# Kernel optimization log

Hardware: AMD Instinct MI355X
Metric: run time of the kernel (lower is better)

Reference implementation:

```python
import jax, jax.numpy as jnp
import numpy as np

N_NODES = 100000
N_EDGES = 1600000
D_IN = 128
D_HID = 64
BN_EPS = 1e-5


def setup_inputs() -> dict:
    key = jax.random.key(0)
    ks = jax.random.split(key, 8)
    x = jax.random.normal(ks[0], (N_NODES, D_IN), dtype=jnp.float32)
    edge_index = jax.random.randint(ks[1], (2, N_EDGES), 0, N_NODES, dtype=jnp.int64)
    # GCNConv1 weight/bias (glorot-ish scale)
    W1 = jax.random.normal(ks[2], (D_IN, D_HID), dtype=jnp.float32) / np.sqrt(D_IN)
    b1 = jnp.zeros((D_HID,), dtype=jnp.float32)
    # BatchNorm1d (eval mode: running stats)
    gamma = jax.random.normal(ks[3], (D_HID,), dtype=jnp.float32) * 0.1 + 1.0
    beta = jax.random.normal(ks[4], (D_HID,), dtype=jnp.float32) * 0.1
    run_mean = jnp.zeros((D_HID,), dtype=jnp.float32)
    run_var = jnp.ones((D_HID,), dtype=jnp.float32)
    # fc1: Linear(2*hidden, 2)
    Wfc = jax.random.normal(ks[5], (2 * D_HID, 2), dtype=jnp.float32) / np.sqrt(2 * D_HID)
    bfc = jnp.zeros((2,), dtype=jnp.float32)
    return {"x": x, "edge_index": edge_index, "W1": W1, "b1": b1,
            "gamma": gamma, "beta": beta, "run_mean": run_mean, "run_var": run_var,
            "Wfc": Wfc, "bfc": bfc}


def gcn_conv(x, edge_index, W, b):
    # PyG GCNConv: add self-loops, symmetric normalization, scatter-add aggregation
    n = x.shape[0]
    loops = jnp.arange(n, dtype=edge_index.dtype)
    row = jnp.concatenate([edge_index[0], loops])  # source nodes
    col = jnp.concatenate([edge_index[1], loops])  # target nodes
    deg = jax.ops.segment_sum(jnp.ones_like(col, dtype=x.dtype), col, num_segments=n)
    dinv = jax.lax.rsqrt(jnp.maximum(deg, 1.0))  # deg >= 1 due to self-loops
    norm = dinv[row] * dinv[col]                 # [E+N]
    h = x @ W                                    # [N, hid]
    msgs = h[row] * norm[:, None]                # gather + scale  [E+N, hid]
    out = jax.ops.segment_sum(msgs, col, num_segments=n)  # scatter-add
    return out + b


def reference(x, edge_index, W1, b1, gamma, beta, run_mean, run_var, Wfc, bfc):
    h = gcn_conv(x, edge_index, W1, b1)
    h = jax.nn.relu(h)
    # dropout(p=0.9) is identity in eval mode
    # BatchNorm1d eval: normalize with running stats
    h = (h - run_mean) * jax.lax.rsqrt(run_var + BN_EPS) * gamma + beta
    h = jax.nn.relu(h)
    # edge gather-concat-linear
    er = jnp.concatenate([h[edge_index[0]], h[edge_index[1]]], axis=1)  # [E, 2*hid]
    return er @ Wfc + bfc  # [E, 2]
```

## Files before the change

### kernel.cpp

```cpp
#include <hip/hip_runtime.h>

#define N_NODES 100000
#define N_EDGES 1600000
#define D_IN 128
#define D_HID 64
#define BN_EPS 1e-5f

#define BUCKET_SHIFT 7
#define BUCKET_W 128
#define N_BUCKETS ((N_NODES + BUCKET_W - 1) / BUCKET_W)
#define N_BIN_BLOCKS 256
#define EDGES_PER_BLOCK (N_EDGES / N_BIN_BLOCKS)
#define GT 2

typedef __attribute__((ext_vector_type(8))) short bf16x8;
typedef __attribute__((ext_vector_type(4))) float f32x4;
typedef __attribute__((ext_vector_type(2))) _Float16 f16x2;
typedef __attribute__((ext_vector_type(4))) _Float16 f16x4;

__device__ __forceinline__ ushort f2bf(float f) {
    unsigned u = __float_as_uint(f);
    u += 0x7FFF + ((u >> 16) & 1);
    return (ushort)(u >> 16);
}

__global__ __launch_bounds__(256) void bin_count_kernel(const int* __restrict__ col,
                                                        int* __restrict__ bcount,
                                                        int* __restrict__ bhist) {
    __shared__ int hist[N_BUCKETS];
    const int t = threadIdx.x;
    for (int i = t; i < N_BUCKETS; i += 256) hist[i] = 0;
    __syncthreads();
    const int e0 = blockIdx.x * EDGES_PER_BLOCK;
    for (int j = t; j < EDGES_PER_BLOCK; j += 256)
        atomicAdd(&hist[col[e0 + j] >> BUCKET_SHIFT], 1);
    __syncthreads();
    for (int i = t; i < N_BUCKETS; i += 256) {
        int h = hist[i];
        bhist[blockIdx.x * N_BUCKETS + i] = h;
        if (h) atomicAdd(&bcount[i], h);
    }
}

__global__ __launch_bounds__(1024) void scan_buckets_kernel(const int* __restrict__ bcount,
                                                            int* __restrict__ bstart,
                                                            int* __restrict__ bcursor,
                                                            int* __restrict__ row_start) {
    __shared__ int tmp[1024];
    int t = threadIdx.x;
    int val = (t < N_BUCKETS) ? bcount[t] : 0;
    tmp[t] = val;
    for (int off = 1; off < 1024; off <<= 1) {
        __syncthreads();
        int add = (t >= off) ? tmp[t - off] : 0;
        __syncthreads();
        tmp[t] += add;
    }
    __syncthreads();
    if (t < N_BUCKETS) {
        int s = tmp[t] - val;
        bstart[t] = s;
        bcursor[t] = s;
    }
    if (t == N_BUCKETS - 1) {
        bstart[N_BUCKETS] = tmp[t];
        row_start[N_NODES] = tmp[t];
    }
}

__global__ __launch_bounds__(256) void bin_scatter_kernel(const int* __restrict__ row,
                                                          const int* __restrict__ col,
                                                          const int* __restrict__ bhist,
                                                          int* __restrict__ bcursor,
                                                          int* __restrict__ binned) {
    __shared__ int hist[N_BUCKETS];
    __shared__ int lbase[N_BUCKETS];
    const int t = threadIdx.x;
    for (int i = t; i < N_BUCKETS; i += 256) {
        int h = bhist[blockIdx.x * N_BUCKETS + i];
        lbase[i] = h ? atomicAdd(&bcursor[i], h) : 0;
        hist[i] = 0;
    }
    __syncthreads();
    const int e0 = blockIdx.x * EDGES_PER_BLOCK;
    for (int j = t; j < EDGES_PER_BLOCK; j += 256) {
        int c = col[e0 + j];
        int r = row[e0 + j];
        int b = c >> BUCKET_SHIFT;
        int rank = atomicAdd(&hist[b], 1);
        binned[lbase[b] + rank] = ((c & (BUCKET_W - 1)) << 17) | r;
    }
}

__global__ __launch_bounds__(256) void bucket_csr_kernel(const int* __restrict__ binned,
                                                         const int* __restrict__ bstart,
                                                         int* __restrict__ csr_src,
                                                         int* __restrict__ row_start,
                                                         float* __restrict__ dinv) {
    __shared__ int hist[BUCKET_W];
    __shared__ int cursor[BUCKET_W];
    const int b = blockIdx.x;
    const int t = threadIdx.x;
    if (t < BUCKET_W) hist[t] = 0;
    __syncthreads();
    const int s = bstart[b], e = bstart[b + 1];
    for (int i = s + t; i < e; i += 256)
        atomicAdd(&hist[binned[i] >> 17], 1);
    __syncthreads();
    if (t < BUCKET_W) cursor[t] = hist[t];
    for (int off = 1; off < BUCKET_W; off <<= 1) {
        __syncthreads();
        int add = (t >= off && t < BUCKET_W) ? cursor[t - off] : 0;
        __syncthreads();
        if (t < BUCKET_W) cursor[t] += add;
    }
    __syncthreads();
    int excl = (t < BUCKET_W) ? (cursor[t] - hist[t]) : 0;
    __syncthreads();
    if (t < BUCKET_W) cursor[t] = excl;
    const int node = b * BUCKET_W + t;
    if (t < BUCKET_W && node < N_NODES) {
        row_start[node] = s + excl;
        dinv[node] = rsqrtf(1.0f + (float)hist[t]);
    }
    __syncthreads();
    for (int i = s + t; i < e; i += 256) {
        int p = binned[i];
        int pos = atomicAdd(&cursor[p >> 17], 1);
        csr_src[s + pos] = p & 0x1FFFF;
    }
}

__global__ __launch_bounds__(256) void gemm_mfma_kernel(const float* __restrict__ x,
                                                        const float* __restrict__ W,
                                                        const float* __restrict__ dinv,
                                                        ushort* __restrict__ h_s) {
    __shared__ ushort xb[16 * 136];
    const int t = threadIdx.x;
    const int l = t & 63;
    const int wv = t >> 6;
    const int q = l >> 4;
    const int m = l & 15;
    bf16x8 bf[4];
    {
        const int n = wv * 16 + m;
        #pragma unroll
        for (int s = 0; s < 4; ++s)
            #pragma unroll
            for (int j = 0; j < 8; ++j)
                bf[s][j] = (short)f2bf(W[(32 * s + 8 * q + j) * D_HID + n]);
    }
    for (int tile = 0; tile < GT; ++tile) {
        const int node0 = blockIdx.x * (16 * GT) + tile * 16;
        __syncthreads();
        for (int i = t; i < 512; i += 256) {
            int r = i >> 5, c4 = i & 31;
            float4 v = *(const float4*)&x[(size_t)(node0 + r) * D_IN + c4 * 4];
            ushort4 u = make_ushort4(f2bf(v.x), f2bf(v.y), f2bf(v.z), f2bf(v.w));
            *(ushort4*)&xb[r * 136 + c4 * 4] = u;
        }
        __syncthreads();
        f32x4 acc = {0.f, 0.f, 0.f, 0.f};
        #pragma unroll
        for (int s = 0; s < 4; ++s) {
            bf16x8 af = *(const bf16x8*)&xb[m * 136 + 32 * s + 8 * q];
            acc = __builtin_amdgcn_mfma_f32_16x16x32_bf16(af, bf[s], acc, 0, 0, 0);
        }
        #pragma unroll
        for (int r = 0; r < 4; ++r) {
            int node = node0 + q * 4 + r;
            _Float16 hv = (_Float16)(acc[r] * dinv[node]);
            h_s[node * D_HID + wv * 16 + m] = __builtin_bit_cast(unsigned short, hv);
        }
    }
}

__global__ __launch_bounds__(256) void aggregate_kernel(const ushort* __restrict__ h_s,
                                                        const float* __restrict__ dinv,
                                                        const int* __restrict__ row_start,
                                                        const int* __restrict__ csr_src,
                                                        const float* __restrict__ b1,
                                                        const float* __restrict__ gamma,
                                                        const float* __restrict__ beta,
                                                        const float* __restrict__ mean,
                                                        const float* __restrict__ var,
                                                        const float* __restrict__ Wfc,
                                                        float4* __restrict__ uv) {
    const f16x4* __restrict__ hsv = (const f16x4*)h_s;
    const int wvid = (blockIdx.x * 256 + threadIdx.x) >> 6;
    const int lane = threadIdx.x & 63;
    const int q = lane >> 4;
    const int ql = lane & 15;
    const int n = wvid * 4 + q;
    f16x4 acc = hsv[n * 16 + ql];
    const int start = row_start[n];
    const int cnt = row_start[n + 1] - start;
    int j = 0;
    for (; j + 8 <= cnt; j += 8) {
        int i0 = csr_src[start + j + 0];
        int i1 = csr_src[start + j + 1];
        int i2 = csr_src[start + j + 2];
        int i3 = csr_src[start + j + 3];
        int i4 = csr_src[start + j + 4];
        int i5 = csr_src[start + j + 5];
        int i6 = csr_src[start + j + 6];
        int i7 = csr_src[start + j + 7];
        f16x4 v0 = hsv[i0 * 16 + ql];
        f16x4 v1 = hsv[i1 * 16 + ql];
        f16x4 v2 = hsv[i2 * 16 + ql];
        f16x4 v3 = hsv[i3 * 16 + ql];
        f16x4 v4 = hsv[i4 * 16 + ql];
        f16x4 v5 = hsv[i5 * 16 + ql];
        f16x4 v6 = hsv[i6 * 16 + ql];
        f16x4 v7 = hsv[i7 * 16 + ql];
        acc += v0; acc += v1; acc += v2; acc += v3;
        acc += v4; acc += v5; acc += v6; acc += v7;
    }
    for (; j + 4 <= cnt; j += 4) {
        int i0 = csr_src[start + j + 0];
        int i1 = csr_src[start + j + 1];
        int i2 = csr_src[start + j + 2];
        int i3 = csr_src[start + j + 3];
        f16x4 v0 = hsv[i0 * 16 + ql];
        f16x4 v1 = hsv[i1 * 16 + ql];
        f16x4 v2 = hsv[i2 * 16 + ql];
        f16x4 v3 = hsv[i3 * 16 + ql];
        acc += v0; acc += v1; acc += v2; acc += v3;
    }
    for (; j + 2 <= cnt; j += 2) {
        int i0 = csr_src[start + j + 0];
        int i1 = csr_src[start + j + 1];
        f16x4 v0 = hsv[i0 * 16 + ql];
        f16x4 v1 = hsv[i1 * 16 + ql];
        acc += v0; acc += v1;
    }
    if (j < cnt)
        acc += hsv[csr_src[start + j] * 16 + ql];
    const float dn = dinv[n];
    float v0 = (float)acc.x * dn;
    float v1 = (float)acc.y * dn;
    float v2 = (float)acc.z * dn;
    float v3 = (float)acc.w * dn;
    float4 bb = *(const float4*)&b1[4 * ql];
    float4 mu = *(const float4*)&mean[4 * ql];
    float4 vr = *(const float4*)&var[4 * ql];
    float4 gm = *(const float4*)&gamma[4 * ql];
    float4 bt = *(const float4*)&beta[4 * ql];
    v0 = fmaxf(v0 + bb.x, 0.f);
    v1 = fmaxf(v1 + bb.y, 0.f);
    v2 = fmaxf(v2 + bb.z, 0.f);
    v3 = fmaxf(v3 + bb.w, 0.f);
    v0 = fmaxf((v0 - mu.x) * rsqrtf(vr.x + BN_EPS) * gm.x + bt.x, 0.f);
    v1 = fmaxf((v1 - mu.y) * rsqrtf(vr.y + BN_EPS) * gm.y + bt.y, 0.f);
    v2 = fmaxf((v2 - mu.z) * rsqrtf(vr.z + BN_EPS) * gm.z + bt.z, 0.f);
    v3 = fmaxf((v3 - mu.w) * rsqrtf(vr.w + BN_EPS) * gm.w + bt.w, 0.f);
    float4 wA = *(const float4*)&Wfc[8 * ql];
    float4 wB = *(const float4*)&Wfc[8 * ql + 4];
    float4 wC = *(const float4*)&Wfc[128 + 8 * ql];
    float4 wD = *(const float4*)&Wfc[128 + 8 * ql + 4];
    float p0 = v0 * wA.x + v1 * wA.z + v2 * wB.x + v3 * wB.z;
    float p1 = v0 * wA.y + v1 * wA.w + v2 * wB.y + v3 * wB.w;
    float p2 = v0 * wC.x + v1 * wC.z + v2 * wD.x + v3 * wD.z;
    float p3 = v0 * wC.y + v1 * wC.w + v2 * wD.y + v3 * wD.w;
    #pragma unroll
    for (int off = 8; off > 0; off >>= 1) {
        p0 += __shfl_xor(p0, off, 64);
        p1 += __shfl_xor(p1, off, 64);
        p2 += __shfl_xor(p2, off, 64);
        p3 += __shfl_xor(p3, off, 64);
    }
    if (ql == 0) uv[n] = make_float4(p0, p1, p2, p3);
}

__global__ __launch_bounds__(256) void edgeout_kernel(const int* __restrict__ row,
                                                      const int* __restrict__ col,
                                                      const float4* __restrict__ uv,
                                                      const float* __restrict__ bfc,
                                                      float2* __restrict__ out) {
    int i = blockIdx.x * 256 + threadIdx.x;
    int e = i * 2;
    int2 rr = *(const int2*)&row[e];
    int2 cc = *(const int2*)&col[e];
    float4 a0 = uv[rr.x];
    float4 b0 = uv[cc.x];
    float4 a1 = uv[rr.y];
    float4 b1 = uv[cc.y];
    float c0 = bfc[0], c1 = bfc[1];
    float4 o = make_float4(a0.x + b0.z + c0, a0.y + b0.w + c1,
                           a1.x + b1.z + c0, a1.y + b1.w + c1);
    *(float4*)&out[e] = o;
}

extern "C" void kernel_launch(void* const* d_in, const int* in_sizes, int n_in,
                              void* d_out, int out_size, void* d_ws, size_t ws_size,
                              hipStream_t stream) {
    const float* x     = (const float*)d_in[0];
    const int*   ei    = (const int*)d_in[1];
    const int*   row   = ei;
    const int*   col   = ei + N_EDGES;
    const float* W1    = (const float*)d_in[2];
    const float* b1    = (const float*)d_in[3];
    const float* gamma = (const float*)d_in[4];
    const float* beta  = (const float*)d_in[5];
    const float* mean  = (const float*)d_in[6];
    const float* var   = (const float*)d_in[7];
    const float* Wfc   = (const float*)d_in[8];
    const float* bfc   = (const float*)d_in[9];
    float2* out = (float2*)d_out;

    char* ws = (char*)d_ws;
    size_t off = 0;
    ushort* h_s      = (ushort*)(ws + off); off += (size_t)N_NODES * D_HID * 2;
    int*   binned    = (int*)(ws + off);    off += (size_t)N_EDGES * 4;
    int*   csr_src   = (int*)(ws + off);    off += (size_t)N_EDGES * 4;
    int*   bhist     = (int*)(ws + off);    off += (size_t)N_BIN_BLOCKS * N_BUCKETS * 4;
    int*   bcount    = (int*)(ws + off);    off += (size_t)(N_BUCKETS + 2) * 4;
    int*   bstart    = (int*)(ws + off);    off += (size_t)(N_BUCKETS + 2) * 4;
    int*   bcursor   = (int*)(ws + off);    off += (size_t)(N_BUCKETS + 2) * 4;
    int*   row_start = (int*)(ws + off);    off += (size_t)(N_NODES + 4) * 4;
    float* dinv      = (float*)(ws + off);  off += (size_t)N_NODES * 4;
    float4* uv       = (float4*)(ws + off); off += (size_t)N_NODES * 16;

    hipMemsetAsync(bcount, 0, (N_BUCKETS + 1) * sizeof(int), stream);
    bin_count_kernel<<<N_BIN_BLOCKS, 256, 0, stream>>>(col, bcount, bhist);
    scan_buckets_kernel<<<1, 1024, 0, stream>>>(bcount, bstart, bcursor, row_start);
    bin_scatter_kernel<<<N_BIN_BLOCKS, 256, 0, stream>>>(row, col, bhist, bcursor, binned);
    bucket_csr_kernel<<<N_BUCKETS, 256, 0, stream>>>(binned, bstart, csr_src, row_start, dinv);
    gemm_mfma_kernel<<<N_NODES / (16 * GT), 256, 0, stream>>>(x, W1, dinv, h_s);
    aggregate_kernel<<<N_NODES / 16, 256, 0, stream>>>(h_s, dinv, row_start, csr_src,
                                                       b1, gamma, beta, mean, var,
                                                       Wfc, uv);
    edgeout_kernel<<<N_EDGES / 512, 256, 0, stream>>>(row, col, uv, bfc, out);
}
```

Before: 219.3 us.

## Replace bucket count/scan passes with fixed-capacity buckets and widen aggregation lanes

```diff
diff --git a/kernel.cpp b/kernel.cpp
--- a/kernel.cpp
+++ b/kernel.cpp
@@ -9,14 +9,14 @@
 #define BUCKET_SHIFT 7
 #define BUCKET_W 128
 #define N_BUCKETS ((N_NODES + BUCKET_W - 1) / BUCKET_W)
+#define BCAP 4096
 #define N_BIN_BLOCKS 256
 #define EDGES_PER_BLOCK (N_EDGES / N_BIN_BLOCKS)
 #define GT 2
 
 typedef __attribute__((ext_vector_type(8))) short bf16x8;
 typedef __attribute__((ext_vector_type(4))) float f32x4;
-typedef __attribute__((ext_vector_type(2))) _Float16 f16x2;
-typedef __attribute__((ext_vector_type(4))) _Float16 f16x4;
+typedef __attribute__((ext_vector_type(8))) _Float16 f16x8;
 
 __device__ __forceinline__ ushort f2bf(float f) {
     unsigned u = __float_as_uint(f);
@@ -24,65 +24,25 @@
     return (ushort)(u >> 16);
 }
 
-__global__ __launch_bounds__(256) void bin_count_kernel(const int* __restrict__ col,
-                                                        int* __restrict__ bcount,
-                                                        int* __restrict__ bhist) {
-    __shared__ int hist[N_BUCKETS];
-    const int t = threadIdx.x;
-    for (int i = t; i < N_BUCKETS; i += 256) hist[i] = 0;
-    __syncthreads();
-    const int e0 = blockIdx.x * EDGES_PER_BLOCK;
-    for (int j = t; j < EDGES_PER_BLOCK; j += 256)
-        atomicAdd(&hist[col[e0 + j] >> BUCKET_SHIFT], 1);
-    __syncthreads();
-    for (int i = t; i < N_BUCKETS; i += 256) {
-        int h = hist[i];
-        bhist[blockIdx.x * N_BUCKETS + i] = h;
-        if (h) atomicAdd(&bcount[i], h);
-    }
-}
-
-__global__ __launch_bounds__(1024) void scan_buckets_kernel(const int* __restrict__ bcount,
-                                                            int* __restrict__ bstart,
-                                                            int* __restrict__ bcursor,
-                                                            int* __restrict__ row_start) {
-    __shared__ int tmp[1024];
-    int t = threadIdx.x;
-    int val = (t < N_BUCKETS) ? bcount[t] : 0;
-    tmp[t] = val;
-    for (int off = 1; off < 1024; off <<= 1) {
-        __syncthreads();
-        int add = (t >= off) ? tmp[t - off] : 0;
-        __syncthreads();
-        tmp[t] += add;
-    }
-    __syncthreads();
-    if (t < N_BUCKETS) {
-        int s = tmp[t] - val;
-        bstart[t] = s;
-        bcursor[t] = s;
-    }
-    if (t == N_BUCKETS - 1) {
-        bstart[N_BUCKETS] = tmp[t];
-        row_start[N_NODES] = tmp[t];
-    }
-}
-
 __global__ __launch_bounds__(256) void bin_scatter_kernel(const int* __restrict__ row,
                                                           const int* __restrict__ col,
-                                                          const int* __restrict__ bhist,
                                                           int* __restrict__ bcursor,
                                                           int* __restrict__ binned) {
     __shared__ int hist[N_BUCKETS];
     __shared__ int lbase[N_BUCKETS];
     const int t = threadIdx.x;
+    for (int i = t; i < N_BUCKETS; i += 256) hist[i] = 0;
+    __syncthreads();
+    const int e0 = blockIdx.x * EDGES_PER_BLOCK;
+    for (int j = t; j < EDGES_PER_BLOCK; j += 256)
+        atomicAdd(&hist[col[e0 + j] >> BUCKET_SHIFT], 1);
+    __syncthreads();
     for (int i = t; i < N_BUCKETS; i += 256) {
-        int h = bhist[blockIdx.x * N_BUCKETS + i];
-        lbase[i] = h ? atomicAdd(&bcursor[i], h) : 0;
+        int h = hist[i];
+        lbase[i] = h ? (i * BCAP + atomicAdd(&bcursor[i], h)) : 0;
         hist[i] = 0;
     }
     __syncthreads();
-    const int e0 = blockIdx.x * EDGES_PER_BLOCK;
     for (int j = t; j < EDGES_PER_BLOCK; j += 256) {
         int c = col[e0 + j];
         int r = row[e0 + j];
@@ -93,9 +53,9 @@
 }
 
 __global__ __launch_bounds__(256) void bucket_csr_kernel(const int* __restrict__ binned,
-                                                         const int* __restrict__ bstart,
+                                                         const int* __restrict__ bcursor,
                                                          int* __restrict__ csr_src,
-                                                         int* __restrict__ row_start,
+                                                         int2* __restrict__ rs2,
                                                          float* __restrict__ dinv) {
     __shared__ int hist[BUCKET_W];
     __shared__ int cursor[BUCKET_W];
@@ -103,7 +63,8 @@
     const int t = threadIdx.x;
     if (t < BUCKET_W) hist[t] = 0;
     __syncthreads();
-    const int s = bstart[b], e = bstart[b + 1];
+    const int s = b * BCAP;
+    const int e = s + bcursor[b];
     for (int i = s + t; i < e; i += 256)
         atomicAdd(&hist[binned[i] >> 17], 1);
     __syncthreads();
@@ -120,7 +81,7 @@
     if (t < BUCKET_W) cursor[t] = excl;
     const int node = b * BUCKET_W + t;
     if (t < BUCKET_W && node < N_NODES) {
-        row_start[node] = s + excl;
+        rs2[node] = make_int2(s + excl, hist[t]);
         dinv[node] = rsqrtf(1.0f + (float)hist[t]);
     }
     __syncthreads();
@@ -177,7 +138,7 @@
 
 __global__ __launch_bounds__(256) void aggregate_kernel(const ushort* __restrict__ h_s,
                                                         const float* __restrict__ dinv,
-                                                        const int* __restrict__ row_start,
+                                                        const int2* __restrict__ rs2,
                                                         const int* __restrict__ csr_src,
                                                         const float* __restrict__ b1,
                                                         const float* __restrict__ gamma,
@@ -186,15 +147,16 @@
                                                         const float* __restrict__ var,
                                                         const float* __restrict__ Wfc,
                                                         float4* __restrict__ uv) {
-    const f16x4* __restrict__ hsv = (const f16x4*)h_s;
+    const f16x8* __restrict__ hsv = (const f16x8*)h_s;
     const int wvid = (blockIdx.x * 256 + threadIdx.x) >> 6;
     const int lane = threadIdx.x & 63;
-    const int q = lane >> 4;
-    const int ql = lane & 15;
-    const int n = wvid * 4 + q;
-    f16x4 acc = hsv[n * 16 + ql];
-    const int start = row_start[n];
-    const int cnt = row_start[n + 1] - start;
+    const int oct = lane >> 3;
+    const int ol = lane & 7;
+    const int n = wvid * 8 + oct;
+    f16x8 acc = hsv[n * 8 + ol];
+    const int2 rs = rs2[n];
+    const int start = rs.x;
+    const int cnt = rs.y;
     int j = 0;
     for (; j + 8 <= cnt; j += 8) {
         int i0 = csr_src[start + j + 0];
@@ -205,14 +167,14 @@
         int i5 = csr_src[start + j + 5];
         int i6 = csr_src[start + j + 6];
         int i7 = csr_src[start + j + 7];
-        f16x4 v0 = hsv[i0 * 16 + ql];
-        f16x4 v1 = hsv[i1 * 16 + ql];
-        f16x4 v2 = hsv[i2 * 16 + ql];
-        f16x4 v3 = hsv[i3 * 16 + ql];
-        f16x4 v4 = hsv[i4 * 16 + ql];
-        f16x4 v5 = hsv[i5 * 16 + ql];
-        f16x4 v6 = hsv[i6 * 16 + ql];
-        f16x4 v7 = hsv[i7 * 16 + ql];
+        f16x8 v0 = hsv[i0 * 8 + ol];
+        f16x8 v1 = hsv[i1 * 8 + ol];
+        f16x8 v2 = hsv[i2 * 8 + ol];
+        f16x8 v3 = hsv[i3 * 8 + ol];
+        f16x8 v4 = hsv[i4 * 8 + ol];
+        f16x8 v5 = hsv[i5 * 8 + ol];
+        f16x8 v6 = hsv[i6 * 8 + ol];
+        f16x8 v7 = hsv[i7 * 8 + ol];
         acc += v0; acc += v1; acc += v2; acc += v3;
         acc += v4; acc += v5; acc += v6; acc += v7;
     }
@@ -221,55 +183,59 @@
         int i1 = csr_src[start + j + 1];
         int i2 = csr_src[start + j + 2];
         int i3 = csr_src[start + j + 3];
-        f16x4 v0 = hsv[i0 * 16 + ql];
-        f16x4 v1 = hsv[i1 * 16 + ql];
-        f16x4 v2 = hsv[i2 * 16 + ql];
-        f16x4 v3 = hsv[i3 * 16 + ql];
+        f16x8 v0 = hsv[i0 * 8 + ol];
+        f16x8 v1 = hsv[i1 * 8 + ol];
+        f16x8 v2 = hsv[i2 * 8 + ol];
+        f16x8 v3 = hsv[i3 * 8 + ol];
         acc += v0; acc += v1; acc += v2; acc += v3;
     }
     for (; j + 2 <= cnt; j += 2) {
         int i0 = csr_src[start + j + 0];
         int i1 = csr_src[start + j + 1];
-        f16x4 v0 = hsv[i0 * 16 + ql];
-        f16x4 v1 = hsv[i1 * 16 + ql];
+        f16x8 v0 = hsv[i0 * 8 + ol];
+        f16x8 v1 = hsv[i1 * 8 + ol];
         acc += v0; acc += v1;
     }
     if (j < cnt)
-        acc += hsv[csr_src[start + j] * 16 + ql];
+        acc += hsv[csr_src[start + j] * 8 + ol];
     const float dn = dinv[n];
-    float v0 = (float)acc.x * dn;
-    float v1 = (float)acc.y * dn;
-    float v2 = (float)acc.z * dn;
-    float v3 = (float)acc.w * dn;
-    float4 bb = *(const float4*)&b1[4 * ql];
-    float4 mu = *(const float4*)&mean[4 * ql];
-    float4 vr = *(const float4*)&var[4 * ql];
-    float4 gm = *(const float4*)&gamma[4 * ql];
-    float4 bt = *(const float4*)&beta[4 * ql];
-    v0 = fmaxf(v0 + bb.x, 0.f);
-    v1 = fmaxf(v1 + bb.y, 0.f);
-    v2 = fmaxf(v2 + bb.z, 0.f);
-    v3 = fmaxf(v3 + bb.w, 0.f);
-    v0 = fmaxf((v0 - mu.x) * rsqrtf(vr.x + BN_EPS) * gm.x + bt.x, 0.f);
-    v1 = fmaxf((v1 - mu.y) * rsqrtf(vr.y + BN_EPS) * gm.y + bt.y, 0.f);
-    v2 = fmaxf((v2 - mu.z) * rsqrtf(vr.z + BN_EPS) * gm.z + bt.z, 0.f);
-    v3 = fmaxf((v3 - mu.w) * rsqrtf(vr.w + BN_EPS) * gm.w + bt.w, 0.f);
-    float4 wA = *(const float4*)&Wfc[8 * ql];
-    float4 wB = *(const float4*)&Wfc[8 * ql + 4];
-    float4 wC = *(const float4*)&Wfc[128 + 8 * ql];
-    float4 wD = *(const float4*)&Wfc[128 + 8 * ql + 4];
-    float p0 = v0 * wA.x + v1 * wA.z + v2 * wB.x + v3 * wB.z;
-    float p1 = v0 * wA.y + v1 * wA.w + v2 * wB.y + v3 * wB.w;
-    float p2 = v0 * wC.x + v1 * wC.z + v2 * wD.x + v3 * wD.z;
-    float p3 = v0 * wC.y + v1 * wC.w + v2 * wD.y + v3 * wD.w;
-    #pragma unroll
-    for (int off = 8; off > 0; off >>= 1) {
+    const int f0 = 8 * ol;
+    float a[8];
+    #pragma unroll
+    for (int k = 0; k < 8; ++k) a[k] = (float)acc[k] * dn;
+    float bb[8], mu[8], vr[8], gm[8], bt[8];
+    *(float4*)&bb[0] = *(const float4*)&b1[f0];    *(float4*)&bb[4] = *(const float4*)&b1[f0 + 4];
+    *(float4*)&mu[0] = *(const float4*)&mean[f0];  *(float4*)&mu[4] = *(const float4*)&mean[f0 + 4];
+    *(float4*)&vr[0] = *(const float4*)&var[f0];   *(float4*)&vr[4] = *(const float4*)&var[f0 + 4];
+    *(float4*)&gm[0] = *(const float4*)&gamma[f0]; *(float4*)&gm[4] = *(const float4*)&gamma[f0 + 4];
+    *(float4*)&bt[0] = *(const float4*)&beta[f0];  *(float4*)&bt[4] = *(const float4*)&beta[f0 + 4];
+    #pragma unroll
+    for (int k = 0; k < 8; ++k) {
+        float v = fmaxf(a[k] + bb[k], 0.f);
+        a[k] = fmaxf((v - mu[k]) * rsqrtf(vr[k] + BN_EPS) * gm[k] + bt[k], 0.f);
+    }
+    float wt[16], wb[16];
+    #pragma unroll
+    for (int k = 0; k < 4; ++k) {
+        *(float4*)&wt[4 * k] = *(const float4*)&Wfc[2 * f0 + 4 * k];
+        *(float4*)&wb[4 * k] = *(const float4*)&Wfc[128 + 2 * f0 + 4 * k];
+    }
+    float p0 = 0.f, p1 = 0.f, p2 = 0.f, p3 = 0.f;
+    #pragma unroll
+    for (int k = 0; k < 8; ++k) {
+        p0 += a[k] * wt[2 * k];
+        p1 += a[k] * wt[2 * k + 1];
+        p2 += a[k] * wb[2 * k];
+        p3 += a[k] * wb[2 * k + 1];
+    }
+    #pragma unroll
+    for (int off = 4; off > 0; off >>= 1) {
         p0 += __shfl_xor(p0, off, 64);
         p1 += __shfl_xor(p1, off, 64);
         p2 += __shfl_xor(p2, off, 64);
         p3 += __shfl_xor(p3, off, 64);
     }
-    if (ql == 0) uv[n] = make_float4(p0, p1, p2, p3);
+    if (ol == 0) uv[n] = make_float4(p0, p1, p2, p3);
 }
 
 __global__ __launch_bounds__(256) void edgeout_kernel(const int* __restrict__ row,
@@ -311,23 +277,18 @@
     char* ws = (char*)d_ws;
     size_t off = 0;
     ushort* h_s      = (ushort*)(ws + off); off += (size_t)N_NODES * D_HID * 2;
-    int*   binned    = (int*)(ws + off);    off += (size_t)N_EDGES * 4;
-    int*   csr_src   = (int*)(ws + off);    off += (size_t)N_EDGES * 4;
-    int*   bhist     = (int*)(ws + off);    off += (size_t)N_BIN_BLOCKS * N_BUCKETS * 4;
-    int*   bcount    = (int*)(ws + off);    off += (size_t)(N_BUCKETS + 2) * 4;
-    int*   bstart    = (int*)(ws + off);    off += (size_t)(N_BUCKETS + 2) * 4;
-    int*   bcursor   = (int*)(ws + off);    off += (size_t)(N_BUCKETS + 2) * 4;
-    int*   row_start = (int*)(ws + off);    off += (size_t)(N_NODES + 4) * 4;
+    int*   binned    = (int*)(ws + off);    off += (size_t)N_BUCKETS * BCAP * 4;
+    int*   csr_src   = (int*)(ws + off);    off += (size_t)N_BUCKETS * BCAP * 4;
+    int*   bcursor   = (int*)(ws + off);    off += ((size_t)N_BUCKETS * 4 + 15) & ~(size_t)15;
+    int2*  rs2       = (int2*)(ws + off);   off += (size_t)N_NODES * 8;
     float* dinv      = (float*)(ws + off);  off += (size_t)N_NODES * 4;
     float4* uv       = (float4*)(ws + off); off += (size_t)N_NODES * 16;
 
-    hipMemsetAsync(bcount, 0, (N_BUCKETS + 1) * sizeof(int), stream);
-    bin_count_kernel<<<N_BIN_BLOCKS, 256, 0, stream>>>(col, bcount, bhist);
-    scan_buckets_kernel<<<1, 1024, 0, stream>>>(bcount, bstart, bcursor, row_start);
-    bin_scatter_kernel<<<N_BIN_BLOCKS, 256, 0, stream>>>(row, col, bhist, bcursor, binned);
-    bucket_csr_kernel<<<N_BUCKETS, 256, 0, stream>>>(binned, bstart, csr_src, row_start, dinv);
+    hipMemsetAsync(bcursor, 0, N_BUCKETS * sizeof(int), stream);
+    bin_scatter_kernel<<<N_BIN_BLOCKS, 256, 0, stream>>>(row, col, bcursor, binned);
+    bucket_csr_kernel<<<N_BUCKETS, 256, 0, stream>>>(binned, bcursor, csr_src, rs2, dinv);
     gemm_mfma_kernel<<<N_NODES / (16 * GT), 256, 0, stream>>>(x, W1, dinv, h_s);
-    aggregate_kernel<<<N_NODES / 16, 256, 0, stream>>>(h_s, dinv, row_start, csr_src,
+    aggregate_kernel<<<N_NODES / 32, 256, 0, stream>>>(h_s, dinv, rs2, csr_src,
                                                        b1, gamma, beta, mean, var,
                                                        Wfc, uv);
     edgeout_kernel<<<N_EDGES / 512, 256, 0, stream>>>(row, col, uv, bfc, out);
```

After: 203.7 us. 1.08x faster.
